# Kernel optimization log

Measured on AMD Instinct MI355X. Metric: run time of the kernel, lower is better.

Reference implementation:

```python
import jax, jax.numpy as jnp
import numpy as np

B, L = 4096, 200
G_DIM, L_DIM, A_DIM, H = 64, 64, 8, 32
MAX_ACTION = 1.0


def _init(k, shape, fan_in):
    bound = 1.0 / np.sqrt(fan_in)
    return jax.random.uniform(k, shape, jnp.float32, -bound, bound)


def setup_inputs() -> dict:
    key = jax.random.key(0)
    ks = jax.random.split(key, 16)
    return dict(
        global_states=jax.random.normal(ks[0], (B, G_DIM), jnp.float32),
        local_states=jax.random.normal(ks[1], (B, L, L_DIM), jnp.float32),
        W_w=_init(ks[2], (H, G_DIM), G_DIM), W_b=_init(ks[3], (H,), G_DIM),
        U_w=_init(ks[4], (H, L_DIM), L_DIM), U_b=_init(ks[5], (H,), L_DIM),
        att_w=_init(ks[6], (1, 2 * H), 2 * H), att_b=_init(ks[7], (1,), 2 * H),
        l1_w=_init(ks[8], (256, 2 * H), 2 * H), l1_b=_init(ks[9], (256,), 2 * H),
        l2_w=_init(ks[10], (256, 256), 256), l2_b=_init(ks[11], (256,), 256),
        l3_w=_init(ks[12], (A_DIM, 256), 256), l3_b=_init(ks[13], (A_DIM,), 256),
    )


def reference(global_states, local_states, W_w, W_b, U_w, U_b,
              att_w, att_b, l1_w, l1_b, l2_w, l2_b, l3_w, l3_b):
    h = W_w.shape[0]  # 32
    wg = global_states @ W_w.T + W_b                              # [B,H]
    ul = jnp.einsum('bld,hd->blh', local_states, U_w) + U_b       # [B,L,H]
    # att input row0 = cat(wg, wg); rows 1..L = cat(wg, ul)
    a_g, a_l = att_w[0, :h], att_w[0, h:]
    g_term = wg @ a_g                                             # [B]
    s0 = jax.nn.leaky_relu(g_term + wg @ a_l + att_b[0])          # [B]
    sl = jax.nn.leaky_relu(g_term[:, None] + ul @ a_l + att_b[0]) # [B,L]
    # normalize by sum (not softmax), matching torch.div(score, score.sum())
    total = s0 + sl.sum(axis=1)                                   # [B]
    n0 = s0 / total                                               # [B]
    nl = sl / total[:, None]                                      # [B,L]
    agg_local = jnp.einsum('bl,blh->bh', nl, ul)                  # [B,H]
    states = jax.nn.relu(jnp.concatenate([n0[:, None] * wg, agg_local], axis=1))  # [B,2H]
    a = jax.nn.relu(states @ l1_w.T + l1_b)
    a = jax.nn.relu(a @ l2_w.T + l2_b)
    a = jax.nn.sigmoid(a @ l3_w.T + l3_b)
    return MAX_ACTION * a
```

## Files before the change

### kernel.cpp

```cpp
#include <hip/hip_runtime.h>
#include <math.h>

#define BB 4096
#define LL 200
#define HH 32
#define PF 8

__global__ __launch_bounds__(256) void actor_fused_kernel(
    const float* __restrict__ gs,
    const float* __restrict__ ls,
    const float* __restrict__ W_w, const float* __restrict__ W_b,
    const float* __restrict__ U_w, const float* __restrict__ U_b,
    const float* __restrict__ att_w, const float* __restrict__ att_b,
    const float* __restrict__ l1_w, const float* __restrict__ l1_b,
    const float* __restrict__ l2_w, const float* __restrict__ l2_b,
    const float* __restrict__ l3_w, const float* __restrict__ l3_b,
    float* __restrict__ out)
{
    __shared__ float c_lds[4 * 64];
    __shared__ float y_lds[4 * 64];
    __shared__ __align__(16) float s_x [4 * 64];
    __shared__ __align__(16) float s_a1[4 * 256];
    __shared__ __align__(16) float s_a2[4 * 260];

    const int tid  = threadIdx.x;
    const int lane = tid & 63;
    const int wid  = tid >> 6;
    const int b    = blockIdx.x * 4 + wid;

    const int h    = lane & 31;
    const int half = lane >> 5;
    const int q    = lane & 15;
    const int lg   = lane >> 4;


    const float4* g4 = (const float4*)(gs + (size_t)b * 64);
    const float4* W4 = (const float4*)(W_w);
    float wg = (half == 0) ? W_b[h] : 0.f;
    #pragma unroll
    for (int dd = 0; dd < 8; ++dd) {
        float4 gv = g4[half * 8 + dd];
        float4 wv = W4[h * 16 + half * 8 + dd];
        wg += gv.x * wv.x + gv.y * wv.y + gv.z * wv.z + gv.w * wv.w;
    }
    wg += __shfl_xor(wg, 32);

    float gt = wg * att_w[h];
    float t2 = wg * att_w[HH + h];
    #pragma unroll
    for (int m = 1; m < 32; m <<= 1) {
        gt += __shfl_xor(gt, m);
        t2 += __shfl_xor(t2, m);
    }
    const float attb = att_b[0];
    const float lin0 = gt + t2 + attb;
    const float s0   = (lin0 > 0.f) ? lin0 : 0.01f * lin0;

    float c = 0.f;
    float ubal = 0.f;
    #pragma unroll
    for (int hh = 0; hh < HH; ++hh) {
        const float alh = att_w[HH + hh];
        c    += alh * U_w[hh * 64 + lane];
        ubal += alh * U_b[hh];
    }
    c_lds[wid * 64 + lane] = c;
    __syncthreads();
    const float4 cq = *(const float4*)&c_lds[wid * 64 + 4 * q];
    const float base = gt + ubal + attb;

    const float4* xs = (const float4*)(ls + (size_t)b * (LL * 64));
    const int idx0 = lg * 16 + q;
    float4 yx = make_float4(0.f, 0.f, 0.f, 0.f);
    float Sacc = 0.f;

    float4 Xbuf[PF];
    #pragma unroll
    for (int i = 0; i < PF; ++i)
        Xbuf[i] = xs[idx0 + i * 64];

    #pragma unroll
    for (int t = 0; t < 50; ++t) {
        float4 X = Xbuf[t & (PF - 1)];
        int tn = t + PF;
        if (tn > 49) tn = 49;
        Xbuf[t & (PF - 1)] = xs[idx0 + tn * 64];

        float p = X.x * cq.x + X.y * cq.y + X.z * cq.z + X.w * cq.w;
        p += __shfl_xor(p, 1);
        p += __shfl_xor(p, 2);
        p += __shfl_xor(p, 4);
        p += __shfl_xor(p, 8);
        const float linv = p + base;
        const float sl = (linv > 0.f) ? linv : 0.01f * linv;
        yx.x += sl * X.x;
        yx.y += sl * X.y;
        yx.z += sl * X.z;
        yx.w += sl * X.w;
        Sacc += sl;
    }

    #pragma unroll
    for (int m = 16; m < 64; m <<= 1) {
        yx.x += __shfl_xor(yx.x, m);
        yx.y += __shfl_xor(yx.y, m);
        yx.z += __shfl_xor(yx.z, m);
        yx.w += __shfl_xor(yx.w, m);
        Sacc += __shfl_xor(Sacc, m);
    }
    if (lane < 16) *(float4*)&y_lds[wid * 64 + 4 * q] = yx;
    __syncthreads();

    float V = (half == 0) ? (U_b[h] * Sacc) : 0.f;
    const float4* U4 = (const float4*)U_w;
    const float4* y4 = (const float4*)&y_lds[wid * 64];
    #pragma unroll
    for (int dd = 0; dd < 8; ++dd) {
        float4 uv = U4[h * 16 + half * 8 + dd];
        float4 yv = y4[half * 8 + dd];
        V += uv.x * yv.x + uv.y * yv.y + uv.z * yv.z + uv.w * yv.w;
    }
    V += __shfl_xor(V, 32);

    const float total = s0 + Sacc;
    const float n0    = s0 / total;
    const float outv  = (lane < 32) ? (n0 * wg) : (V / total);
    s_x[wid * 64 + lane] = fmaxf(outv, 0.f);
    __syncthreads();


    float w[64];

    {
        const float* wr = l1_w + tid * 64;
        #pragma unroll
        for (int d = 0; d < 64; ++d) w[d] = wr[d];
        float bias = l1_b[tid];
        #pragma unroll
        for (int r = 0; r < 4; ++r) {
            float acc = bias;
            #pragma unroll
            for (int d = 0; d < 64; ++d)
                acc += s_x[r * 64 + d] * w[d];
            s_a1[r * 256 + tid] = fmaxf(acc, 0.f);
        }
    }
    __syncthreads();

    {
        float acc[4];
        float bias = l2_b[tid];
        #pragma unroll
        for (int r = 0; r < 4; ++r) acc[r] = bias;
        for (int kc = 0; kc < 4; ++kc) {
            const float* wr = l2_w + tid * 256 + kc * 64;
            #pragma unroll
            for (int d = 0; d < 64; ++d) w[d] = wr[d];
            #pragma unroll
            for (int r = 0; r < 4; ++r) {
                #pragma unroll
                for (int d = 0; d < 64; ++d)
                    acc[r] += s_a1[r * 256 + kc * 64 + d] * w[d];
            }
        }
        #pragma unroll
        for (int r = 0; r < 4; ++r)
            s_a2[r * 260 + tid] = fmaxf(acc[r], 0.f);
    }
    __syncthreads();

    if (tid < 32) {
        int r = tid >> 3, o = tid & 7;
        float acc = l3_b[o];
        const float4* wr4 = (const float4*)(l3_w + o * 256);
        const float4* a4  = (const float4*)&s_a2[r * 260];
        #pragma unroll 8
        for (int k = 0; k < 64; ++k) {
            float4 av = a4[k];
            float4 wv = wr4[k];
            acc += av.x * wv.x + av.y * wv.y + av.z * wv.z + av.w * wv.w;
        }
        out[(size_t)(blockIdx.x * 4 + r) * 8 + o] =
            1.f / (1.f + __expf(-acc));
    }
}

extern "C" void kernel_launch(void* const* d_in, const int* in_sizes, int n_in,
                              void* d_out, int out_size, void* d_ws, size_t ws_size,
                              hipStream_t stream)
{
    const float* gs    = (const float*)d_in[0];
    const float* ls    = (const float*)d_in[1];
    const float* W_w   = (const float*)d_in[2];
    const float* W_b   = (const float*)d_in[3];
    const float* U_w   = (const float*)d_in[4];
    const float* U_b   = (const float*)d_in[5];
    const float* att_w = (const float*)d_in[6];
    const float* att_b = (const float*)d_in[7];
    const float* l1_w  = (const float*)d_in[8];
    const float* l1_b  = (const float*)d_in[9];
    const float* l2_w  = (const float*)d_in[10];
    const float* l2_b  = (const float*)d_in[11];
    const float* l3_w  = (const float*)d_in[12];
    const float* l3_b  = (const float*)d_in[13];

    actor_fused_kernel<<<BB / 4, 256, 0, stream>>>(
        gs, ls, W_w, W_b, U_w, U_b, att_w, att_b,
        l1_w, l1_b, l2_w, l2_b, l3_w, l3_b, (float*)d_out);
}
```

Before: 354.5 us.

## Split fused kernel into streaming attention kernel and separate MLP kernel

```diff
diff --git a/kernel.cpp b/kernel.cpp
--- a/kernel.cpp
+++ b/kernel.cpp
@@ -5,6 +5,206 @@
 #define LL 200
 #define HH 32
 #define PF 8
+
+
+__global__ __launch_bounds__(128, 8) void actor_stream_kernel(
+    const float* __restrict__ gs,
+    const float* __restrict__ ls,
+    const float* __restrict__ W_w, const float* __restrict__ W_b,
+    const float* __restrict__ U_w, const float* __restrict__ U_b,
+    const float* __restrict__ att_w, const float* __restrict__ att_b,
+    float* __restrict__ states)
+{
+    __shared__ float c_lds[64];
+    __shared__ __align__(16) float y_part[2][64];
+    __shared__ float S_part[2];
+    __shared__ __align__(16) float y_lds[64];
+
+    const int tid  = threadIdx.x;
+    const int lane = tid & 63;
+    const int wid  = tid >> 6;
+    const int b    = blockIdx.x;
+
+    const int h    = lane & 31;
+    const int half = lane >> 5;
+
+    const float4* g4 = (const float4*)(gs + (size_t)b * 64);
+    const float4* W4 = (const float4*)(W_w);
+    float wg = (half == 0) ? W_b[h] : 0.f;
+    #pragma unroll
+    for (int dd = 0; dd < 8; ++dd) {
+        float4 gv = g4[half * 8 + dd];
+        float4 wv = W4[h * 16 + half * 8 + dd];
+        wg += gv.x * wv.x + gv.y * wv.y + gv.z * wv.z + gv.w * wv.w;
+    }
+    wg += __shfl_xor(wg, 32);
+
+    float gt = wg * att_w[h];
+    float t2 = wg * att_w[HH + h];
+    #pragma unroll
+    for (int m = 1; m < 32; m <<= 1) {
+        gt += __shfl_xor(gt, m);
+        t2 += __shfl_xor(t2, m);
+    }
+    const float attb = att_b[0];
+    const float lin0 = gt + t2 + attb;
+    const float s0   = (lin0 > 0.f) ? lin0 : 0.01f * lin0;
+
+    float c = 0.f;
+    float ubal = 0.f;
+    #pragma unroll
+    for (int hh = 0; hh < HH; ++hh) {
+        const float alh = att_w[HH + hh];
+        c    += alh * U_w[hh * 64 + lane];
+        ubal += alh * U_b[hh];
+    }
+    if (wid == 0) c_lds[lane] = c;
+    __syncthreads();
+    const int q = lane & 15;
+    const float4 cq = *(const float4*)&c_lds[4 * q];
+    const float base = gt + ubal + attb;
+
+    const float4* xs = (const float4*)(ls + (size_t)b * (LL * 64)) + wid * 1600;
+    float4 yx = make_float4(0.f, 0.f, 0.f, 0.f);
+    float Sacc = 0.f;
+
+    float4 Xbuf[PF];
+    #pragma unroll
+    for (int i = 0; i < PF; ++i)
+        Xbuf[i] = xs[lane + i * 64];
+
+    #pragma unroll
+    for (int t = 0; t < 25; ++t) {
+        float4 X = Xbuf[t & (PF - 1)];
+        int tn = t + PF;
+        if (tn > 24) tn = 24;
+        Xbuf[t & (PF - 1)] = xs[lane + tn * 64];
+
+        float p = X.x * cq.x + X.y * cq.y + X.z * cq.z + X.w * cq.w;
+        p += __shfl_xor(p, 1);
+        p += __shfl_xor(p, 2);
+        p += __shfl_xor(p, 4);
+        p += __shfl_xor(p, 8);
+        const float linv = p + base;
+        const float sl = (linv > 0.f) ? linv : 0.01f * linv;
+        yx.x += sl * X.x;
+        yx.y += sl * X.y;
+        yx.z += sl * X.z;
+        yx.w += sl * X.w;
+        Sacc += sl;
+    }
+
+    #pragma unroll
+    for (int m = 16; m < 64; m <<= 1) {
+        yx.x += __shfl_xor(yx.x, m);
+        yx.y += __shfl_xor(yx.y, m);
+        yx.z += __shfl_xor(yx.z, m);
+        yx.w += __shfl_xor(yx.w, m);
+        Sacc += __shfl_xor(Sacc, m);
+    }
+    if (lane < 16) *(float4*)&y_part[wid][4 * q] = yx;
+    if (lane == 0) S_part[wid] = Sacc;
+    __syncthreads();
+
+    if (tid < 16) {
+        float4 ya = *(const float4*)&y_part[0][4 * tid];
+        float4 yb = *(const float4*)&y_part[1][4 * tid];
+        ya.x += yb.x; ya.y += yb.y; ya.z += yb.z; ya.w += yb.w;
+        *(float4*)&y_lds[4 * tid] = ya;
+    }
+    __syncthreads();
+
+    if (wid == 0) {
+        const float Stot = S_part[0] + S_part[1];
+        float V = (half == 0) ? (U_b[h] * Stot) : 0.f;
+        const float4* U4 = (const float4*)U_w;
+        const float4* y4 = (const float4*)y_lds;
+        #pragma unroll
+        for (int dd = 0; dd < 8; ++dd) {
+            float4 uv = U4[h * 16 + half * 8 + dd];
+            float4 yv = y4[half * 8 + dd];
+            V += uv.x * yv.x + uv.y * yv.y + uv.z * yv.z + uv.w * yv.w;
+        }
+        V += __shfl_xor(V, 32);
+
+        const float total = s0 + Stot;
+        const float n0    = s0 / total;
+        const float outv  = (lane < 32) ? (n0 * wg) : (V / total);
+        states[(size_t)b * 64 + lane] = fmaxf(outv, 0.f);
+    }
+}
+
+__global__ __launch_bounds__(256) void actor_mlp_kernel(
+    const float* __restrict__ states,
+    const float* __restrict__ l1_w, const float* __restrict__ l1_b,
+    const float* __restrict__ l2_w, const float* __restrict__ l2_b,
+    const float* __restrict__ l3_w, const float* __restrict__ l3_b,
+    float* __restrict__ out)
+{
+    __shared__ __align__(16) float s_x [4 * 64];
+    __shared__ __align__(16) float s_a1[4 * 256];
+    __shared__ __align__(16) float s_a2[4 * 260];
+
+    const int tid = threadIdx.x;
+
+    s_x[tid] = states[(size_t)blockIdx.x * 256 + tid];
+    __syncthreads();
+
+    float w[64];
+
+    {
+        const float* wr = l1_w + tid * 64;
+        #pragma unroll
+        for (int d = 0; d < 64; ++d) w[d] = wr[d];
+        float bias = l1_b[tid];
+        #pragma unroll
+        for (int r = 0; r < 4; ++r) {
+            float acc = bias;
+            #pragma unroll
+            for (int d = 0; d < 64; ++d)
+                acc += s_x[r * 64 + d] * w[d];
+            s_a1[r * 256 + tid] = fmaxf(acc, 0.f);
+        }
+    }
+    __syncthreads();
+
+    {
+        float acc[4];
+        float bias = l2_b[tid];
+        #pragma unroll
+        for (int r = 0; r < 4; ++r) acc[r] = bias;
+        for (int kc = 0; kc < 4; ++kc) {
+            const float* wr = l2_w + tid * 256 + kc * 64;
+            #pragma unroll
+            for (int d = 0; d < 64; ++d) w[d] = wr[d];
+            #pragma unroll
+            for (int r = 0; r < 4; ++r) {
+                #pragma unroll
+                for (int d = 0; d < 64; ++d)
+                    acc[r] += s_a1[r * 256 + kc * 64 + d] * w[d];
+            }
+        }
+        #pragma unroll
+        for (int r = 0; r < 4; ++r)
+            s_a2[r * 260 + tid] = fmaxf(acc[r], 0.f);
+    }
+    __syncthreads();
+
+    if (tid < 32) {
+        int r = tid >> 3, o = tid & 7;
+        float acc = l3_b[o];
+        const float4* wr4 = (const float4*)(l3_w + o * 256);
+        const float4* a4  = (const float4*)&s_a2[r * 260];
+        #pragma unroll 8
+        for (int k = 0; k < 64; ++k) {
+            float4 av = a4[k];
+            float4 wv = wr4[k];
+            acc += av.x * wv.x + av.y * wv.y + av.z * wv.z + av.w * wv.w;
+        }
+        out[(size_t)(blockIdx.x * 4 + r) * 8 + o] =
+            1.f / (1.f + __expf(-acc));
+    }
+}
 
 __global__ __launch_bounds__(256) void actor_fused_kernel(
     const float* __restrict__ gs,
@@ -33,7 +233,6 @@
     const int q    = lane & 15;
     const int lg   = lane >> 4;
 
-
     const float4* g4 = (const float4*)(gs + (size_t)b * 64);
     const float4* W4 = (const float4*)(W_w);
     float wg = (half == 0) ? W_b[h] : 0.f;
@@ -128,9 +327,7 @@
     s_x[wid * 64 + lane] = fmaxf(outv, 0.f);
     __syncthreads();
 
-
     float w[64];
-
     {
         const float* wr = l1_w + tid * 64;
         #pragma unroll
@@ -146,7 +343,6 @@
         }
     }
     __syncthreads();
-
     {
         float acc[4];
         float bias = l2_b[tid];
@@ -204,7 +400,16 @@
     const float* l3_w  = (const float*)d_in[12];
     const float* l3_b  = (const float*)d_in[13];
 
-    actor_fused_kernel<<<BB / 4, 256, 0, stream>>>(
-        gs, ls, W_w, W_b, U_w, U_b, att_w, att_b,
-        l1_w, l1_b, l2_w, l2_b, l3_w, l3_b, (float*)d_out);
+    const size_t need = (size_t)BB * 64 * sizeof(float);
+    if (d_ws != nullptr && ws_size >= need) {
+        float* states = (float*)d_ws;
+        actor_stream_kernel<<<BB, 128, 0, stream>>>(
+            gs, ls, W_w, W_b, U_w, U_b, att_w, att_b, states);
+        actor_mlp_kernel<<<BB / 4, 256, 0, stream>>>(
+            states, l1_w, l1_b, l2_w, l2_b, l3_w, l3_b, (float*)d_out);
+    } else {
+        actor_fused_kernel<<<BB / 4, 256, 0, stream>>>(
+            gs, ls, W_w, W_b, U_w, U_b, att_w, att_b,
+            l1_w, l1_b, l2_w, l2_b, l3_w, l3_b, (float*)d_out);
+    }
 }
```

New measurement: 399.1 us. 12.6% more time.

## Stream local states through LDS with async global_load_lds double buffering

Applied to the files above, without the earlier changes.

```diff
diff --git a/kernel.cpp b/kernel.cpp
--- a/kernel.cpp
+++ b/kernel.cpp
@@ -4,7 +4,18 @@
 #define BB 4096
 #define LL 200
 #define HH 32
-#define PF 8
+
+
+__device__ __forceinline__ void issue_group5(const float* src_lane,
+                                             float* lds_dst)
+{
+    #pragma unroll
+    for (int cc = 0; cc < 5; ++cc)
+        __builtin_amdgcn_global_load_lds(
+            (__attribute__((address_space(1))) const void*)(src_lane + cc * 256),
+            (__attribute__((address_space(3))) void*)(lds_dst + cc * 256),
+            16, 0, 0);
+}
 
 __global__ __launch_bounds__(256) void actor_fused_kernel(
     const float* __restrict__ gs,
@@ -17,8 +28,9 @@
     const float* __restrict__ l3_w, const float* __restrict__ l3_b,
     float* __restrict__ out)
 {
-    __shared__ float c_lds[4 * 64];
-    __shared__ float y_lds[4 * 64];
+    __shared__ __align__(16) float stage[4][2][1280];
+    __shared__ float c_lds[64];
+    __shared__ __align__(16) float y_lds[4][64];
     __shared__ __align__(16) float s_x [4 * 64];
     __shared__ __align__(16) float s_a1[4 * 256];
     __shared__ __align__(16) float s_a2[4 * 260];
@@ -31,7 +43,6 @@
     const int h    = lane & 31;
     const int half = lane >> 5;
     const int q    = lane & 15;
-    const int lg   = lane >> 4;
 
 
     const float4* g4 = (const float4*)(gs + (size_t)b * 64);
@@ -64,40 +75,51 @@
         c    += alh * U_w[hh * 64 + lane];
         ubal += alh * U_b[hh];
     }
-    c_lds[wid * 64 + lane] = c;
-    __syncthreads();
-    const float4 cq = *(const float4*)&c_lds[wid * 64 + 4 * q];
+    c_lds[lane] = c;
+    __syncthreads();
+    const float4 cq = *(const float4*)&c_lds[4 * q];
     const float base = gt + ubal + attb;
 
-    const float4* xs = (const float4*)(ls + (size_t)b * (LL * 64));
-    const int idx0 = lg * 16 + q;
+    const float* rowp = ls + (size_t)b * (LL * 64);
+    float* bufA = &stage[wid][0][0];
+    float* bufB = &stage[wid][1][0];
+
+    asm volatile("s_waitcnt vmcnt(0)" ::: "memory");
+
+    issue_group5(rowp + 0 * 1280 + (lane << 2), bufA);
+    issue_group5(rowp + 1 * 1280 + (lane << 2), bufB);
+
     float4 yx = make_float4(0.f, 0.f, 0.f, 0.f);
     float Sacc = 0.f;
 
-    float4 Xbuf[PF];
-    #pragma unroll
-    for (int i = 0; i < PF; ++i)
-        Xbuf[i] = xs[idx0 + i * 64];
-
-    #pragma unroll
-    for (int t = 0; t < 50; ++t) {
-        float4 X = Xbuf[t & (PF - 1)];
-        int tn = t + PF;
-        if (tn > 49) tn = 49;
-        Xbuf[t & (PF - 1)] = xs[idx0 + tn * 64];
-
-        float p = X.x * cq.x + X.y * cq.y + X.z * cq.z + X.w * cq.w;
-        p += __shfl_xor(p, 1);
-        p += __shfl_xor(p, 2);
-        p += __shfl_xor(p, 4);
-        p += __shfl_xor(p, 8);
-        const float linv = p + base;
-        const float sl = (linv > 0.f) ? linv : 0.01f * linv;
-        yx.x += sl * X.x;
-        yx.y += sl * X.y;
-        yx.z += sl * X.z;
-        yx.w += sl * X.w;
-        Sacc += sl;
+    #pragma unroll
+    for (int g = 0; g < 10; ++g) {
+        const float* cur = (g & 1) ? bufB : bufA;
+        if (g < 9) asm volatile("s_waitcnt vmcnt(5)" ::: "memory");
+        else       asm volatile("s_waitcnt vmcnt(0)" ::: "memory");
+        __builtin_amdgcn_sched_barrier(0);
+
+        #pragma unroll
+        for (int cc = 0; cc < 5; ++cc) {
+            float4 X = ((const float4*)cur)[cc * 64 + lane];
+            float p = X.x * cq.x + X.y * cq.y + X.z * cq.z + X.w * cq.w;
+            p += __shfl_xor(p, 1);
+            p += __shfl_xor(p, 2);
+            p += __shfl_xor(p, 4);
+            p += __shfl_xor(p, 8);
+            const float linv = p + base;
+            const float sl = (linv > 0.f) ? linv : 0.01f * linv;
+            yx.x += sl * X.x;
+            yx.y += sl * X.y;
+            yx.z += sl * X.z;
+            yx.w += sl * X.w;
+            Sacc += sl;
+        }
+
+        __builtin_amdgcn_sched_barrier(0);
+        if (g < 8)
+            issue_group5(rowp + (g + 2) * 1280 + (lane << 2),
+                         (g & 1) ? bufB : bufA);
     }
 
     #pragma unroll
@@ -108,12 +130,12 @@
         yx.w += __shfl_xor(yx.w, m);
         Sacc += __shfl_xor(Sacc, m);
     }
-    if (lane < 16) *(float4*)&y_lds[wid * 64 + 4 * q] = yx;
+    if (lane < 16) *(float4*)&y_lds[wid][4 * q] = yx;
     __syncthreads();
 
     float V = (half == 0) ? (U_b[h] * Sacc) : 0.f;
     const float4* U4 = (const float4*)U_w;
-    const float4* y4 = (const float4*)&y_lds[wid * 64];
+    const float4* y4 = (const float4*)&y_lds[wid][0];
     #pragma unroll
     for (int dd = 0; dd < 8; ++dd) {
         float4 uv = U4[h * 16 + half * 8 + dd];
```

Result: slower. 395.3 us (+11.5%).

## Restructure MLP layers to use coalesced float4 weight loads with shuffle reductions

Applied to the files above, without the earlier changes.

```diff
diff --git a/kernel.cpp b/kernel.cpp
--- a/kernel.cpp
+++ b/kernel.cpp
@@ -5,6 +5,7 @@
 #define LL 200
 #define HH 32
 #define PF 8
+
 
 __global__ __launch_bounds__(256) void actor_fused_kernel(
     const float* __restrict__ gs,
@@ -128,44 +129,51 @@
     s_x[wid * 64 + lane] = fmaxf(outv, 0.f);
     __syncthreads();
 
-
-    float w[64];
+    const int rg = lane >> 4;
+    const int kl = lane & 15;
+    const int u0 = wid * 64;
 
     {
-        const float* wr = l1_w + tid * 64;
-        #pragma unroll
-        for (int d = 0; d < 64; ++d) w[d] = wr[d];
-        float bias = l1_b[tid];
-        #pragma unroll
-        for (int r = 0; r < 4; ++r) {
-            float acc = bias;
-            #pragma unroll
-            for (int d = 0; d < 64; ++d)
-                acc += s_x[r * 64 + d] * w[d];
-            s_a1[r * 256 + tid] = fmaxf(acc, 0.f);
+        const float4 xv = *(const float4*)(s_x + rg * 64 + kl * 4);
+        #pragma unroll 8
+        for (int i = 0; i < 64; ++i) {
+            const int u = u0 + i;
+            const float4 wv = *(const float4*)(l1_w + u * 64 + kl * 4);
+            float acc = wv.x * xv.x + wv.y * xv.y + wv.z * xv.z + wv.w * xv.w;
+            acc += __shfl_xor(acc, 1);
+            acc += __shfl_xor(acc, 2);
+            acc += __shfl_xor(acc, 4);
+            acc += __shfl_xor(acc, 8);
+            if (kl == 0)
+                s_a1[rg * 256 + u] = fmaxf(acc + l1_b[u], 0.f);
         }
     }
     __syncthreads();
 
     {
-        float acc[4];
-        float bias = l2_b[tid];
-        #pragma unroll
-        for (int r = 0; r < 4; ++r) acc[r] = bias;
-        for (int kc = 0; kc < 4; ++kc) {
-            const float* wr = l2_w + tid * 256 + kc * 64;
-            #pragma unroll
-            for (int d = 0; d < 64; ++d) w[d] = wr[d];
-            #pragma unroll
-            for (int r = 0; r < 4; ++r) {
-                #pragma unroll
-                for (int d = 0; d < 64; ++d)
-                    acc[r] += s_a1[r * 256 + kc * 64 + d] * w[d];
-            }
+        const float4 av0 = *(const float4*)(s_a1 + rg * 256 +   0 + kl * 4);
+        const float4 av1 = *(const float4*)(s_a1 + rg * 256 +  64 + kl * 4);
+        const float4 av2 = *(const float4*)(s_a1 + rg * 256 + 128 + kl * 4);
+        const float4 av3 = *(const float4*)(s_a1 + rg * 256 + 192 + kl * 4);
+        #pragma unroll 4
+        for (int i = 0; i < 64; ++i) {
+            const int u = u0 + i;
+            const float4* wr = (const float4*)(l2_w + (size_t)u * 256);
+            const float4 w0v = wr[     kl];
+            const float4 w1v = wr[16 + kl];
+            const float4 w2v = wr[32 + kl];
+            const float4 w3v = wr[48 + kl];
+            float acc = w0v.x * av0.x + w0v.y * av0.y + w0v.z * av0.z + w0v.w * av0.w;
+            acc      += w1v.x * av1.x + w1v.y * av1.y + w1v.z * av1.z + w1v.w * av1.w;
+            acc      += w2v.x * av2.x + w2v.y * av2.y + w2v.z * av2.z + w2v.w * av2.w;
+            acc      += w3v.x * av3.x + w3v.y * av3.y + w3v.z * av3.z + w3v.w * av3.w;
+            acc += __shfl_xor(acc, 1);
+            acc += __shfl_xor(acc, 2);
+            acc += __shfl_xor(acc, 4);
+            acc += __shfl_xor(acc, 8);
+            if (kl == 0)
+                s_a2[rg * 260 + u] = fmaxf(acc + l2_b[u], 0.f);
         }
-        #pragma unroll
-        for (int r = 0; r < 4; ++r)
-            s_a2[r * 260 + tid] = fmaxf(acc[r], 0.f);
     }
     __syncthreads();
 
```

New measurement: 448.9 us. 26.6% more time.
